# Kernel optimization log

Measured on AMD Instinct MI355X. Metric: run time of the kernel, lower is better.

The kernel has to match this reference:

```python
import jax, jax.numpy as jnp
import numpy as np

N = 8192          # number of samples (atoms)
D_IN = 256        # in_features (descriptor dim)
D_OUT = 256       # out_features
NUM_TYPE = 64     # number of atom types
INIT_VAL = 0.01


def setup_inputs() -> dict:
    key = jax.random.key(0)
    k1, k2, k3, k4 = jax.random.split(key, 4)
    batch_i = jax.random.randint(k1, (N,), 0, NUM_TYPE)                     # [N] type index per sample
    batch_descriptor = jax.random.normal(k2, (N, D_IN), dtype=jnp.float32)  # [N, D_IN]
    layer1 = INIT_VAL * jax.random.normal(k3, (NUM_TYPE, D_OUT, D_IN), dtype=jnp.float32)
    W = INIT_VAL * jax.random.normal(k4, (D_OUT, D_IN), dtype=jnp.float32)  # linear_adjust.weight
    b = jnp.zeros((D_OUT,), dtype=jnp.float32)                              # linear_adjust.bias (init 0)
    return {"batch_i": batch_i, "batch_descriptor": batch_descriptor,
            "layer1": layer1, "W": W, "b": b}


def reference(batch_i, batch_descriptor, layer1, W, b):
    # Per-sample type-indexed weight gather + batched mat-vec (torch.bmm)
    # layer1[batch_i]: [N, D_OUT, D_IN]; descriptor: [N, D_IN] -> [N, D_OUT]
    gathered = layer1[batch_i]
    out = jnp.einsum('noi,ni->no', gathered, batch_descriptor)
    out = jnp.tanh(out)  # ACT assumed tanh (undefined in snippet)
    # linear_adjust: x @ W.T + b
    adjust = batch_descriptor @ W.T + b
    return out + adjust
```

## Files before the change

kernel.cpp:

```cpp
#include <hip/hip_runtime.h>
#include <cstddef>

#define NUM_TYPE 64
#define DD 256
#define NN 8192
#define GM64 192
#define PSTR 264

typedef __bf16 bf16x8 __attribute__((ext_vector_type(8)));
typedef __bf16 bf16x4 __attribute__((ext_vector_type(4)));
typedef float f32x4 __attribute__((ext_vector_type(4)));

__device__ __forceinline__ bf16x4 cvt4(float4 v) {
  bf16x4 h;
  h[0] = (__bf16)v.x; h[1] = (__bf16)v.y; h[2] = (__bf16)v.z; h[3] = (__bf16)v.w;
  return h;
}

__device__ __forceinline__ float tanh_fast(float x) {
  float xc = fminf(fmaxf(x, -15.f), 15.f);
  float e = __expf(2.f * xc);
  return (e - 1.f) / (e + 1.f);
}

__global__ __launch_bounds__(1024) void perm_conv(
    const int* __restrict__ bi,
    const float* __restrict__ desc,
    const float* __restrict__ W,
    int* __restrict__ type_off, int* __restrict__ perm,
    __bf16* __restrict__ descB, __bf16* __restrict__ Wb) {
  const int b = blockIdx.x;
  const int tid = threadIdx.x;
  if (b == 0) {
    __shared__ int wcnt[16][NUM_TYPE];
    __shared__ int wbase[16][NUM_TYPE];
    __shared__ int cnt[NUM_TYPE];
    __shared__ int tstart[NUM_TYPE];
    __shared__ int totals[1];
    const int w = tid >> 6;
    for (int i = tid; i < 16 * NUM_TYPE; i += 1024) ((int*)wcnt)[i] = 0;
    __syncthreads();
    int myv[8];
#pragma unroll
    for (int rnd = 0; rnd < 8; ++rnd) {
      int v = bi[rnd * 1024 + tid];
      myv[rnd] = v;
      atomicAdd(&wcnt[w][v], 1);
    }
    __syncthreads();
    if (tid < NUM_TYPE) {
      int s = 0;
#pragma unroll
      for (int ww = 0; ww < 16; ++ww) { wbase[ww][tid] = s; s += wcnt[ww][tid]; }
      cnt[tid] = s;
    }
    __syncthreads();
    if (tid == 0) {
      int s = 0;
      for (int t = 0; t < NUM_TYPE; ++t) { tstart[t] = s; s += cnt[t]; }
      totals[0] = s;
    }
    __syncthreads();
    if (tid < NUM_TYPE) {
      const int s0 = tstart[tid];
      type_off[tid] = s0;
#pragma unroll
      for (int ww = 0; ww < 16; ++ww) wbase[ww][tid] += s0;
    }
    if (tid == 0) type_off[NUM_TYPE] = totals[0];
    __syncthreads();
#pragma unroll
    for (int rnd = 0; rnd < 8; ++rnd) {
      int v = myv[rnd];
      int p = atomicAdd(&wbase[w][v], 1);
      perm[p] = rnd * 1024 + tid;
    }
  } else {
    const float4* srcD = reinterpret_cast<const float4*>(desc);
    const float4* srcW = reinterpret_cast<const float4*>(W);
#pragma unroll
    for (int it = 0; it < 2; ++it) {
      const int idx = (b - 1) * 2048 + it * 1024 + tid;
      if (idx < 524288)
        *reinterpret_cast<bf16x4*>(descB + (size_t)idx * 4) = cvt4(srcD[idx]);
      else
        *reinterpret_cast<bf16x4*>(Wb + (size_t)(idx - 524288) * 4) = cvt4(srcW[idx - 524288]);
    }
  }
}

__global__ __launch_bounds__(512, 2) void gemm_res32(
    const __bf16* __restrict__ descB,
    const float* __restrict__ layer1,
    const __bf16* __restrict__ Wb,
    const float* __restrict__ bias,
    const int* __restrict__ type_off,
    const int* __restrict__ perm,
    float* __restrict__ out) {
  extern __shared__ __bf16 lds[];
  __bf16* At = lds;
  __bf16* Ll = lds + 64 * PSTR;
  __bf16* Wl = lds + 96 * PSTR;

  const int d = blockIdx.x;
  const int t = (d & 7) + 8 * ((d >> 3) & 7);
  const int cb = d >> 6;
  const int off = type_off[t];
  const int limit = type_off[t + 1];
  const int cnt = limit - off;
  if (cnt <= 0) return;
  const int ngr = (cnt + 63) >> 6;

  const int tid = threadIdx.x;
  const int wid = tid >> 6;
  const int lane = tid & 63;
  const int l15 = lane & 15;
  const int lg = lane >> 4;
  const int wr = wid >> 1;
  const int wc = wid & 1;

  {
    const float* Lsrc = layer1 + ((size_t)t * DD + cb * 32) * DD;
#pragma unroll
    for (int it = 0; it < 4; ++it) {
      const int idx = it * 512 + tid;
      const int col = idx >> 6, seg = idx & 63;
      *reinterpret_cast<bf16x4*>(Ll + col * PSTR + seg * 4) =
          cvt4(*reinterpret_cast<const float4*>(Lsrc + (size_t)col * DD + seg * 4));
    }
    const __bf16* Wsrc = Wb + (size_t)(cb * 32) * DD;
#pragma unroll
    for (int it = 0; it < 2; ++it) {
      const int idx = it * 512 + tid;
      const int col = idx >> 5, seg = idx & 31;
      *reinterpret_cast<bf16x8*>(Wl + col * PSTR + seg * 8) =
          *reinterpret_cast<const bf16x8*>(Wsrc + (size_t)col * DD + seg * 8);
    }
  }

  const int colg = cb * 32 + wc * 16 + l15;
  const float bv = bias[colg];

  for (int j = 0; j < ngr; ++j) {
    const int first = off + j * 64;
    if (j > 0) __syncthreads();
#pragma unroll
    for (int it = 0; it < 4; ++it) {
      const int idx = it * 512 + tid;
      const int row = idx >> 5, seg = idx & 31;
      const int rr = first + row;
      bf16x8 v = {};
      if (rr < limit) v = *reinterpret_cast<const bf16x8*>(descB + (size_t)perm[rr] * DD + seg * 8);
      *reinterpret_cast<bf16x8*>(At + row * PSTR + seg * 8) = v;
    }
    __syncthreads();

    f32x4 accL = {0.f, 0.f, 0.f, 0.f};
    f32x4 accW = {0.f, 0.f, 0.f, 0.f};
#pragma unroll
    for (int kc = 0; kc < 8; ++kc) {
      bf16x8 af = *reinterpret_cast<const bf16x8*>(At + (wr * 16 + l15) * PSTR + kc * 32 + lg * 8);
      bf16x8 bl = *reinterpret_cast<const bf16x8*>(Ll + (wc * 16 + l15) * PSTR + kc * 32 + lg * 8);
      bf16x8 bw = *reinterpret_cast<const bf16x8*>(Wl + (wc * 16 + l15) * PSTR + kc * 32 + lg * 8);
      accL = __builtin_amdgcn_mfma_f32_16x16x32_bf16(af, bl, accL, 0, 0, 0);
      accW = __builtin_amdgcn_mfma_f32_16x16x32_bf16(af, bw, accW, 0, 0, 0);
    }

    const int orow = first + wr * 16 + l15;
    const int sOut = (orow < limit) ? perm[orow] : -1;
#pragma unroll
    for (int i = 0; i < 4; ++i) {
      const int sv = __shfl(sOut, lg * 4 + i, 64);
      if (sv >= 0)
        __builtin_nontemporal_store(tanh_fast(accL[i]) + accW[i] + bv,
                                    out + (size_t)sv * DD + colg);
    }
  }
}

extern "C" void kernel_launch(void* const* d_in, const int* in_sizes, int n_in,
                              void* d_out, int out_size, void* d_ws, size_t ws_size,
                              hipStream_t stream) {
  const int* bi       = (const int*)d_in[0];
  const float* desc   = (const float*)d_in[1];
  const float* layer1 = (const float*)d_in[2];
  const float* W      = (const float*)d_in[3];
  const float* bias   = (const float*)d_in[4];
  float* out = (float*)d_out;

  char* ws = (char*)d_ws;
  int* type_off = (int*)(ws);
  int* perm     = (int*)(ws + 8192);
  __bf16* descB = (__bf16*)(ws + 65536);
  __bf16* Wb    = (__bf16*)(ws + 65536 + 4194304);

  const int ldsBytes = 128 * PSTR * 2;

  hipLaunchKernelGGL(perm_conv, dim3(265), dim3(1024), 0, stream,
                     bi, desc, W, type_off, perm, descB, Wb);
  hipLaunchKernelGGL(gemm_res32, dim3(512), dim3(512), ldsBytes, stream,
                     descB, layer1, Wb, bias, type_off, perm, out);
}
```

Before: 25.65 us.

## Load gathered descriptor rows directly to LDS with XOR swizzle and cached perm

Replaces the register-staged gather of descriptor rows into padded LDS with global_load_lds direct-to-LDS loads, using an unpadded layout with an XOR swizzle to avoid bank conflicts. The per-type permutation indices are cached in LDS so repeated perm lookups avoid global memory. Tail rows are clamped to the last valid row instead of being zero-filled. This is meant to cut VGPR traffic and load latency in the gather, but there is no double buffering, and each group still waits for all loads to finish before computing.

Result: faster. 23.83 us, median of 2 (-7.1%).

```diff
diff --git a/kernel.cpp b/kernel.cpp
--- a/kernel.cpp
+++ b/kernel.cpp
@@ -4,8 +4,8 @@
 #define NUM_TYPE 64
 #define DD 256
 #define NN 8192
-#define GM64 192
 #define PSTR 264
+#define PT 512
 
 typedef __bf16 bf16x8 __attribute__((ext_vector_type(8)));
 typedef __bf16 bf16x4 __attribute__((ext_vector_type(4)));
@@ -99,8 +99,9 @@
     float* __restrict__ out) {
   extern __shared__ __bf16 lds[];
   __bf16* At = lds;
-  __bf16* Ll = lds + 64 * PSTR;
-  __bf16* Wl = lds + 96 * PSTR;
+  __bf16* Ll = lds + 64 * DD;
+  __bf16* Wl = Ll + 32 * PSTR;
+  int* ptile = (int*)(Wl + 32 * PSTR);
 
   const int d = blockIdx.x;
   const int t = (d & 7) + 8 * ((d >> 3) & 7);
@@ -119,6 +120,8 @@
   const int wr = wid >> 1;
   const int wc = wid & 1;
 
+  for (int i = tid; i < cnt && i < PT; i += 512) ptile[i] = perm[off + i];
+
   {
     const float* Lsrc = layer1 + ((size_t)t * DD + cb * 32) * DD;
 #pragma unroll
@@ -137,37 +140,51 @@
           *reinterpret_cast<const bf16x8*>(Wsrc + (size_t)col * DD + seg * 8);
     }
   }
+  __syncthreads();
 
   const int colg = cb * 32 + wc * 16 + l15;
   const float bv = bias[colg];
 
+#define A_ISSUE(firstLocal)                                                   \
+  {                                                                           \
+    _Pragma("unroll")                                                         \
+    for (int it = 0; it < 4; ++it) {                                          \
+      const int r0 = wid * 8 + it * 2;                                        \
+      const int row = r0 + (lane >> 5);                                       \
+      int lr = (firstLocal) + row;                                            \
+      if (lr >= cnt) lr = cnt - 1;                                            \
+      const int pv = (lr < PT) ? ptile[lr] : perm[off + lr];                  \
+      const int segg = (lane & 31) ^ (row & 7);                               \
+      const __bf16* gsrc = descB + (size_t)pv * DD + segg * 8;                \
+      __builtin_amdgcn_global_load_lds(                                       \
+          (const __attribute__((address_space(1))) void*)gsrc,                \
+          (__attribute__((address_space(3))) void*)(At + r0 * DD),            \
+          16, 0, 0);                                                          \
+    }                                                                         \
+  }
+
+  A_ISSUE(0)
+  asm volatile("s_waitcnt vmcnt(0)" ::: "memory");
+  __syncthreads();
+
   for (int j = 0; j < ngr; ++j) {
-    const int first = off + j * 64;
-    if (j > 0) __syncthreads();
-#pragma unroll
-    for (int it = 0; it < 4; ++it) {
-      const int idx = it * 512 + tid;
-      const int row = idx >> 5, seg = idx & 31;
-      const int rr = first + row;
-      bf16x8 v = {};
-      if (rr < limit) v = *reinterpret_cast<const bf16x8*>(descB + (size_t)perm[rr] * DD + seg * 8);
-      *reinterpret_cast<bf16x8*>(At + row * PSTR + seg * 8) = v;
-    }
-    __syncthreads();
-
+    const int rowA = wr * 16 + l15;
+    const int rsw = rowA & 7;
     f32x4 accL = {0.f, 0.f, 0.f, 0.f};
     f32x4 accW = {0.f, 0.f, 0.f, 0.f};
 #pragma unroll
     for (int kc = 0; kc < 8; ++kc) {
-      bf16x8 af = *reinterpret_cast<const bf16x8*>(At + (wr * 16 + l15) * PSTR + kc * 32 + lg * 8);
+      const int c0 = (kc * 4 + lg) ^ rsw;
+      bf16x8 af = *reinterpret_cast<const bf16x8*>(At + rowA * DD + c0 * 8);
       bf16x8 bl = *reinterpret_cast<const bf16x8*>(Ll + (wc * 16 + l15) * PSTR + kc * 32 + lg * 8);
       bf16x8 bw = *reinterpret_cast<const bf16x8*>(Wl + (wc * 16 + l15) * PSTR + kc * 32 + lg * 8);
       accL = __builtin_amdgcn_mfma_f32_16x16x32_bf16(af, bl, accL, 0, 0, 0);
       accW = __builtin_amdgcn_mfma_f32_16x16x32_bf16(af, bw, accW, 0, 0, 0);
     }
 
-    const int orow = first + wr * 16 + l15;
-    const int sOut = (orow < limit) ? perm[orow] : -1;
+    const int olr = j * 64 + rowA;
+    int sOut = -1;
+    if (olr < cnt) sOut = (olr < PT) ? ptile[olr] : perm[off + olr];
 #pragma unroll
     for (int i = 0; i < 4; ++i) {
       const int sv = __shfl(sOut, lg * 4 + i, 64);
@@ -175,7 +192,15 @@
         __builtin_nontemporal_store(tanh_fast(accL[i]) + accW[i] + bv,
                                     out + (size_t)sv * DD + colg);
     }
-  }
+
+    if (j + 1 < ngr) {
+      __syncthreads();
+      A_ISSUE((j + 1) * 64)
+      asm volatile("s_waitcnt vmcnt(0)" ::: "memory");
+      __syncthreads();
+    }
+  }
+#undef A_ISSUE
 }
 
 extern "C" void kernel_launch(void* const* d_in, const int* in_sizes, int n_in,
@@ -194,7 +219,7 @@
   __bf16* descB = (__bf16*)(ws + 65536);
   __bf16* Wb    = (__bf16*)(ws + 65536 + 4194304);
 
-  const int ldsBytes = 128 * PSTR * 2;
+  const int ldsBytes = 64 * DD * 2 + 2 * 32 * PSTR * 2 + PT * 4;
 
   hipLaunchKernelGGL(perm_conv, dim3(265), dim3(1024), 0, stream,
                      bi, desc, W, type_off, perm, descB, Wb);
```
